# Kernel optimization log

Measured on AMD Instinct MI355X. Metric: run time of the kernel, lower is better.

Reference implementation:

```python
import jax, jax.numpy as jnp
import numpy as np

CAPACITY_FACTOR = 2  # GShard top-2 gating: C = 2*S/E


def setup_inputs() -> dict:
    key = jax.random.key(0)
    k1, k2, k3, k4 = jax.random.split(key, 4)
    B, T, M, E, F = 4, 1024, 1024, 8, 4096
    x = jax.random.normal(k1, (B, T, M), dtype=jnp.float32)
    wg = jax.random.normal(k2, (M, E), dtype=jnp.float32) * 0.02
    w1 = jax.random.normal(k3, (E, M, F), dtype=jnp.float32) * 0.02
    w2 = jax.random.normal(k4, (E, F, M), dtype=jnp.float32) * 0.02
    return {"x": x, "wg": wg, "w1": w1, "w2": w2}


def top2_gate(xs, wg):
    # xs: [S, M] tokens; wg: [M, E] gate projection.
    S = xs.shape[0]
    E = wg.shape[1]
    C = CAPACITY_FACTOR * S // E  # expert capacity
    logits = xs @ wg                                  # [S, E]
    gates = jax.nn.softmax(logits, axis=-1)           # [S, E]
    # top-1 expert
    idx1 = jnp.argmax(gates, axis=-1)                 # [S]
    mask1 = jax.nn.one_hot(idx1, E, dtype=jnp.int32)  # [S, E]
    # top-2 expert: mask out top-1 and take argmax again
    logits_no1 = jnp.where(mask1.astype(bool), -jnp.inf, logits)
    idx2 = jnp.argmax(logits_no1, axis=-1)
    mask2 = jax.nn.one_hot(idx2, E, dtype=jnp.int32)
    # positions within each expert's buffer (cumsum over tokens)
    loc1 = jnp.cumsum(mask1, axis=0) - 1              # [S, E]
    loc2 = jnp.cumsum(mask2, axis=0) - 1 + jnp.sum(mask1, axis=0, keepdims=True)
    # load-balancing auxiliary loss
    me = jnp.mean(gates, axis=0)
    ce = jnp.mean(mask1.astype(gates.dtype), axis=0)
    l_aux = jnp.mean(me * ce) * (E * E)
    # drop tokens beyond capacity
    mask1 = mask1 * (loc1 < C)
    mask2 = mask2 * (loc2 < C)
    loc1_s = jnp.sum(loc1 * mask1, axis=1)            # [S] slot of token in its top-1 expert
    loc2_s = jnp.sum(loc2 * mask2, axis=1)
    mask1f = mask1.astype(gates.dtype)
    mask2f = mask2.astype(gates.dtype)
    gates1_s = jnp.sum(gates * mask1f, axis=1)
    gates2_s = jnp.sum(gates * mask2f, axis=1)
    denom = gates1_s + gates2_s
    denom = jnp.where(denom < 1e-9, 1e-9, denom)
    g1 = gates1_s / denom
    g2 = gates2_s / denom
    # combine weights [S, E, C]
    combine = (g1[:, None] * mask1f)[:, :, None] * jax.nn.one_hot(loc1_s, C, dtype=gates.dtype)[:, None, :] \
            + (g2[:, None] * mask2f)[:, :, None] * jax.nn.one_hot(loc2_s, C, dtype=gates.dtype)[:, None, :]
    dispatch = (combine > 0).astype(gates.dtype)      # one-hot dispatch mask [S, E, C]
    return l_aux, combine, dispatch


def reference(x, wg, w1, w2):
    B, T, M = x.shape
    xs = x.reshape(-1, M)                                  # [S, M]
    l_aux, combine_weights, dispatch_mask = top2_gate(xs, wg)
    # dispatch: one-hot matmul (E*C x S) @ (S x M) -> [E, C, M]
    dispatched = jnp.einsum('sec,sm->ecm', dispatch_mask, xs)
    # per-expert FFN (relu)
    h = jax.nn.relu(jnp.einsum('ecm,emf->ecf', dispatched, w1))
    expert_out = jnp.einsum('ecf,efm->ecm', h, w2)         # [E, C, M]
    # combine: (S x E*C) @ (E*C x M) -> [S, M]
    combined = jnp.einsum('sec,ecm->sm', combine_weights, expert_out)
    return combined.reshape(B, T, M), l_aux
```

## Files before the change

kernel.cpp:

```cpp
#include <hip/hip_runtime.h>
#include <hip/hip_bf16.h>

typedef unsigned short u16;
typedef short bf16x8 __attribute__((ext_vector_type(8)));
typedef float f32x4 __attribute__((ext_vector_type(4)));
typedef u16 u16x8 __attribute__((ext_vector_type(8)));

#define S_TOK 4096
#define MDIM 1024
#define EDIM 8
#define FDIM 4096
#define CCAP 1024
#define HALF_F 2048

__device__ __align__(16) u16   g_xb [S_TOK * MDIM];
__device__ __align__(16) u16   g_wT [EDIM * FDIM * MDIM];
__device__ __align__(16) u16   g_h  [EDIM * CCAP * FDIM];
__device__ __align__(16) float g_eo [2 * EDIM * CCAP * MDIM];
__device__ float g_gates[S_TOK * EDIM];
__device__ int   g_idx1[S_TOK], g_idx2[S_TOK];
__device__ int   g_loc1[S_TOK], g_loc2[S_TOK];
__device__ float g_tg1[S_TOK],  g_tg2[S_TOK];
__device__ int   g_ts1[S_TOK],  g_ts2[S_TOK];
__device__ int   g_slot[EDIM * CCAP];

__device__ __forceinline__ u16 f2bf(float f) {
    union { float f; unsigned u; } c; c.f = f;
    unsigned r = c.u + 0x7FFFu + ((c.u >> 16) & 1u);
    return (u16)(r >> 16);
}
__device__ __forceinline__ void async16(const void* g, void* l) {
    __builtin_amdgcn_global_load_lds(
        (const __attribute__((address_space(1))) unsigned int*)g,
        (__attribute__((address_space(3))) unsigned int*)l, 16, 0, 0);
}

__global__ void cvt_x(const float* __restrict__ x) {
    int i = (blockIdx.x * 256 + threadIdx.x) * 8;
    float4 a = *(const float4*)(x + i);
    float4 b = *(const float4*)(x + i + 4);
    u16x8 o;
    o[0] = f2bf(a.x); o[1] = f2bf(a.y); o[2] = f2bf(a.z); o[3] = f2bf(a.w);
    o[4] = f2bf(b.x); o[5] = f2bf(b.y); o[6] = f2bf(b.z); o[7] = f2bf(b.w);
    *(u16x8*)(g_xb + i) = o;
}

__global__ void gate_kernel(const float* __restrict__ x, const float* __restrict__ wg) {
    __shared__ float wgT[EDIM * MDIM];
    const int tid = threadIdx.x, wave = tid >> 6, lane = tid & 63;
    for (int i = tid; i < EDIM * MDIM; i += 256) {
        int e = i >> 10, m = i & 1023;
        wgT[i] = wg[m * EDIM + e];
    }
    __syncthreads();
    const int s = blockIdx.x * 4 + wave;
    const float* xr = x + (size_t)s * MDIM;
    float lg[EDIM];
#pragma unroll
    for (int e = 0; e < EDIM; e++) lg[e] = 0.f;
#pragma unroll
    for (int j = 0; j < 4; j++) {
        int m0 = j * 256 + lane * 4;
        float4 xv = *(const float4*)(xr + m0);
#pragma unroll
        for (int e = 0; e < EDIM; e++) {
            float4 wv = *(const float4*)(&wgT[e * MDIM + m0]);
            lg[e] += xv.x * wv.x + xv.y * wv.y + xv.z * wv.z + xv.w * wv.w;
        }
    }
#pragma unroll
    for (int e = 0; e < EDIM; e++) {
        float v = lg[e];
        for (int o = 32; o >= 1; o >>= 1) v += __shfl_xor(v, o);
        lg[e] = v;
    }
    if (lane == 0) {
        float mx = lg[0];
#pragma unroll
        for (int e = 1; e < EDIM; e++) mx = fmaxf(mx, lg[e]);
        float ex[EDIM], sum = 0.f;
#pragma unroll
        for (int e = 0; e < EDIM; e++) { ex[e] = expf(lg[e] - mx); sum += ex[e]; }
        int i1 = 0; float b1 = lg[0];
#pragma unroll
        for (int e = 1; e < EDIM; e++) if (lg[e] > b1) { b1 = lg[e]; i1 = e; }
        int i2 = -1; float b2 = -3.4e38f;
#pragma unroll
        for (int e = 0; e < EDIM; e++) if (e != i1 && lg[e] > b2) { b2 = lg[e]; i2 = e; }
        float inv = 1.f / sum;
#pragma unroll
        for (int e = 0; e < EDIM; e++) g_gates[s * EDIM + e] = ex[e] * inv;
        g_idx1[s] = i1; g_idx2[s] = i2;
    }
}

__global__ void scan_kernel(float* __restrict__ out_laux) {
    __shared__ float me_sh[EDIM];
    __shared__ int cnt_sh[EDIM];
    const int t = threadIdx.x, wave = t >> 6, lane = t & 63;
    if (t < EDIM) { me_sh[t] = 0.f; cnt_sh[t] = 0; }
    for (int i = t; i < EDIM * CCAP; i += 1024) g_slot[i] = -1;
    __syncthreads();
    float lm[EDIM]; int lc[EDIM];
#pragma unroll
    for (int e = 0; e < EDIM; e++) { lm[e] = 0.f; lc[e] = 0; }
    for (int j = 0; j < 4; j++) {
        int s = t + 1024 * j;
        const float* g = g_gates + (size_t)s * EDIM;
        int i1 = g_idx1[s];
#pragma unroll
        for (int e = 0; e < EDIM; e++) { lm[e] += g[e]; lc[e] += (i1 == e); }
    }
#pragma unroll
    for (int e = 0; e < EDIM; e++) {
        float v = lm[e]; int c = lc[e];
        for (int o = 32; o >= 1; o >>= 1) { v += __shfl_xor(v, o); c += __shfl_xor(c, o); }
        if (lane == 0) { atomicAdd(&me_sh[e], v); atomicAdd(&cnt_sh[e], c); }
    }
    __syncthreads();
    {
        int e = wave & 7;
        const int* idx = (wave < 8) ? g_idx1 : g_idx2;
        int* loc = (wave < 8) ? g_loc1 : g_loc2;
        int running = (wave < 8) ? 0 : cnt_sh[e];
        for (int s0 = 0; s0 < S_TOK; s0 += 64) {
            int v = idx[s0 + lane];
            bool f = (v == e);
            unsigned long long m = __ballot(f);
            int rank = __popcll(m & ((1ull << lane) - 1ull));
            if (f) loc[s0 + lane] = running + rank;
            running += __popcll(m);
        }
    }
    __syncthreads();
    for (int j = 0; j < 4; j++) {
        int s = t + 1024 * j;
        int e1 = g_idx1[s], e2 = g_idx2[s];
        int l1 = g_loc1[s], l2 = g_loc2[s];
        bool k1 = l1 < CCAP, k2 = l2 < CCAP;
        float G1 = k1 ? g_gates[s * EDIM + e1] : 0.f;
        float G2 = k2 ? g_gates[s * EDIM + e2] : 0.f;
        float den = G1 + G2; den = den < 1e-9f ? 1e-9f : den;
        g_tg1[s] = G1 / den; g_tg2[s] = G2 / den;
        g_ts1[s] = k1 ? (e1 * CCAP + l1) : -1;
        g_ts2[s] = k2 ? (e2 * CCAP + l2) : -1;
        if (k1) g_slot[e1 * CCAP + l1] = s;
        if (k2) g_slot[e2 * CCAP + l2] = s;
    }
    if (t == 0) {
        float la = 0.f;
        for (int e = 0; e < EDIM; e++)
            la += (me_sh[e] / (float)S_TOK) * ((float)cnt_sh[e] / (float)S_TOK);
        la *= (float)EDIM;
        out_laux[0] = la;
    }
}

template <int R, int C>
__global__ void transpose_cvt(const float* __restrict__ in) {
    __shared__ __align__(16) u16 t[64][72];
    const float* I = in + (size_t)blockIdx.z * R * C;
    u16* O = g_wT + (size_t)blockIdx.z * R * C;
    const int tid = threadIdx.x;
    const int c0 = blockIdx.x * 64, r0 = blockIdx.y * 64;
    const int rr = tid >> 4;
    const int cc = (tid & 15) * 4;
#pragma unroll
    for (int j = 0; j < 4; j++) {
        int r = rr + j * 16;
        float4 v = *(const float4*)(I + (size_t)(r0 + r) * C + c0 + cc);
        t[cc + 0][r] = f2bf(v.x);
        t[cc + 1][r] = f2bf(v.y);
        t[cc + 2][r] = f2bf(v.z);
        t[cc + 3][r] = f2bf(v.w);
    }
    __syncthreads();
    const int oc = tid >> 2;
    const int orr = (tid & 3) * 16;
    u16x8 a = *(const u16x8*)(&t[oc][orr]);
    u16x8 b = *(const u16x8*)(&t[oc][orr + 8]);
    u16* dst = O + (size_t)(c0 + oc) * R + r0 + orr;
    *(u16x8*)(dst) = a;
    *(u16x8*)(dst + 8) = b;
}

__global__ void gemm_gather() {
    constexpr int K = MDIM, N = FDIM;
    __shared__ __align__(16) u16 As[128 * 32];
    __shared__ __align__(16) u16 Bs[128 * 32];
    const int tid = threadIdx.x, wave = tid >> 6, lane = tid & 63;
    const int e = blockIdx.z, qr = tid >> 2, qc = tid & 3;
    const int sb = e * CCAP + blockIdx.y * 128;
    int t0 = g_slot[sb + qr];      if (t0 < 0) t0 = 0;
    int t1 = g_slot[sb + 64 + qr]; if (t1 < 0) t1 = 0;
    const u16* ga0 = g_xb + (size_t)t0 * K + qc * 8;
    const u16* ga1 = g_xb + (size_t)t1 * K + qc * 8;
    const u16* B = g_wT + (size_t)e * N * K + (size_t)(blockIdx.x * 128) * K;
    const u16* gb0 = B + (size_t)qr * K + qc * 8;
    const u16* gb1 = gb0 + (size_t)64 * K;
    u16* lA0 = As + wave * 512;
    u16* lA1 = As + 2048 + wave * 512;
    u16* lB0 = Bs + wave * 512;
    u16* lB1 = Bs + 2048 + wave * 512;

    f32x4 acc[4][4];
#pragma unroll
    for (int i = 0; i < 4; i++)
#pragma unroll
        for (int j = 0; j < 4; j++) { f32x4 z = {0.f, 0.f, 0.f, 0.f}; acc[i][j] = z; }
    const int wm = (wave >> 1) * 64, wn = (wave & 1) * 64;
    const int lrow = lane & 15, lq = lane >> 4;

    for (int k0 = 0; k0 < K; k0 += 32) {
        __syncthreads();
        async16(ga0, lA0); async16(ga1, lA1);
        async16(gb0, lB0); async16(gb1, lB1);
        ga0 += 32; ga1 += 32; gb0 += 32; gb1 += 32;
        __syncthreads();
        bf16x8 af[4], bfr[4];
#pragma unroll
    for (int i = 0; i < 4; i++)
            af[i] = *(const bf16x8*)(As + (wm + i * 16 + lrow) * 32 + lq * 8);
#pragma unroll
        for (int i = 0; i < 4; i++)
            bfr[i] = *(const bf16x8*)(Bs + (wn + i * 16 + lrow) * 32 + lq * 8);
#pragma unroll
        for (int mi = 0; mi < 4; mi++)
#pragma unroll
            for (int ni = 0; ni < 4; ni++)
                acc[mi][ni] = __builtin_amdgcn_mfma_f32_16x16x32_bf16(
                    af[mi], bfr[ni], acc[mi][ni], 0, 0, 0);
    }
    const int r0 = blockIdx.y * 128 + wm + lq * 4;
    const int c0 = blockIdx.x * 128 + wn + lrow;
    u16* D = g_h + (size_t)e * CCAP * N;
#pragma unroll
    for (int mi = 0; mi < 4; mi++)
#pragma unroll
        for (int v = 0; v < 4; v++) {
            size_t r = (size_t)(r0 + mi * 16 + v) * N;
#pragma unroll
            for (int ni = 0; ni < 4; ni++) {
                float xv = acc[mi][ni][v];
                xv = xv > 0.f ? xv : 0.f;
                D[r + c0 + ni * 16] = f2bf(xv);
            }
        }
}

__global__ void gemm_bt() {
    constexpr int LD = FDIM;
    constexpr int K = HALF_F;
    constexpr int N = MDIM;
    __shared__ __align__(16) u16 As[128 * 32];
    __shared__ __align__(16) u16 Bs[128 * 32];
    const int tid = threadIdx.x, wave = tid >> 6, lane = tid & 63;
    const int e = blockIdx.z >> 1, ks = blockIdx.z & 1;
    const int qr = tid >> 2, qc = tid & 3;
    const u16* A = g_h + (size_t)e * CCAP * LD + (size_t)(blockIdx.y * 128) * LD + ks * K;
    const u16* B = g_wT + (size_t)e * N * LD + (size_t)(blockIdx.x * 128) * LD + ks * K;
    const u16* ga0 = A + (size_t)qr * LD + qc * 8;
    const u16* ga1 = ga0 + (size_t)64 * LD;
    const u16* gb0 = B + (size_t)qr * LD + qc * 8;
    const u16* gb1 = gb0 + (size_t)64 * LD;
    u16* lA0 = As + wave * 512;
    u16* lA1 = As + 2048 + wave * 512;
    u16* lB0 = Bs + wave * 512;
    u16* lB1 = Bs + 2048 + wave * 512;

    f32x4 acc[4][4];
#pragma unroll
    for (int i = 0; i < 4; i++)
#pragma unroll
        for (int j = 0; j < 4; j++) { f32x4 z = {0.f, 0.f, 0.f, 0.f}; acc[i][j] = z; }
    const int wm = (wave >> 1) * 64, wn = (wave & 1) * 64;
    const int lrow = lane & 15, lq = lane >> 4;

    for (int k0 = 0; k0 < K; k0 += 32) {
        __syncthreads();
        async16(ga0, lA0); async16(ga1, lA1);
        async16(gb0, lB0); async16(gb1, lB1);
        ga0 += 32; ga1 += 32; gb0 += 32; gb1 += 32;
        __syncthreads();
        bf16x8 af[4], bfr[4];
#pragma unroll
        for (int i = 0; i < 4; i++)
            af[i] = *(const bf16x8*)(As + (wm + i * 16 + lrow) * 32 + lq * 8);
#pragma unroll
        for (int i = 0; i < 4; i++)
            bfr[i] = *(const bf16x8*)(Bs + (wn + i * 16 + lrow) * 32 + lq * 8);
#pragma unroll
        for (int mi = 0; mi < 4; mi++)
#pragma unroll
            for (int ni = 0; ni < 4; ni++)
                acc[mi][ni] = __builtin_amdgcn_mfma_f32_16x16x32_bf16(
                    af[mi], bfr[ni], acc[mi][ni], 0, 0, 0);
    }
    const int r0 = blockIdx.y * 128 + wm + lq * 4;
    const int c0 = blockIdx.x * 128 + wn + lrow;
    float* D = g_eo + (size_t)ks * (EDIM * CCAP * MDIM) + (size_t)e * CCAP * N;
#pragma unroll
    for (int mi = 0; mi < 4; mi++)
#pragma unroll
        for (int v = 0; v < 4; v++) {
            size_t r = (size_t)(r0 + mi * 16 + v) * N;
#pragma unroll
            for (int ni = 0; ni < 4; ni++)
                D[r + c0 + ni * 16] = acc[mi][ni][v];
        }
}

__global__ void combine_kernel(float* __restrict__ out) {
    const int s = blockIdx.x, t = threadIdx.x;
    constexpr size_t HALF = (size_t)EDIM * CCAP * MDIM;
    float g1 = g_tg1[s], g2 = g_tg2[s];
    int p1 = g_ts1[s], p2 = g_ts2[s];
    float a0 = 0.f, a1 = 0.f, a2 = 0.f, a3 = 0.f;
    if (p1 >= 0) {
        float4 v = ((const float4*)(g_eo + (size_t)p1 * MDIM))[t];
        float4 w = ((const float4*)(g_eo + HALF + (size_t)p1 * MDIM))[t];
        a0 = g1 * (v.x + w.x); a1 = g1 * (v.y + w.y);
        a2 = g1 * (v.z + w.z); a3 = g1 * (v.w + w.w);
    }
    if (p2 >= 0) {
        float4 v = ((const float4*)(g_eo + (size_t)p2 * MDIM))[t];
        float4 w = ((const float4*)(g_eo + HALF + (size_t)p2 * MDIM))[t];
        a0 += g2 * (v.x + w.x); a1 += g2 * (v.y + w.y);
        a2 += g2 * (v.z + w.z); a3 += g2 * (v.w + w.w);
    }
    float4 o; o.x = a0; o.y = a1; o.z = a2; o.w = a3;
    ((float4*)out)[(size_t)s * 256 + t] = o;
}

extern "C" void kernel_launch(void* const* d_in, const int* in_sizes, int n_in,
                              void* d_out, int out_size, void* d_ws, size_t ws_size,
                              hipStream_t stream) {
    const float* x  = (const float*)d_in[0];
    const float* wg = (const float*)d_in[1];
    const float* w1 = (const float*)d_in[2];
    const float* w2 = (const float*)d_in[3];
    float* out = (float*)d_out;

    cvt_x<<<dim3(S_TOK * MDIM / 2048), 256, 0, stream>>>(x);
    gate_kernel<<<dim3(S_TOK / 4), 256, 0, stream>>>(x, wg);
    scan_kernel<<<dim3(1), 1024, 0, stream>>>(out + 4194304);

    transpose_cvt<MDIM, FDIM><<<dim3(FDIM / 64, MDIM / 64, EDIM), 256, 0, stream>>>(w1);
    gemm_gather<<<dim3(FDIM / 128, CCAP / 128, EDIM), 256, 0, stream>>>();

    transpose_cvt<FDIM, MDIM><<<dim3(MDIM / 64, FDIM / 64, EDIM), 256, 0, stream>>>(w2);
    gemm_bt<<<dim3(MDIM / 128, CCAP / 128, EDIM * 2), 256, 0, stream>>>();

    combine_kernel<<<dim3(S_TOK), 256, 0, stream>>>(out);
}
```

Baseline: 555.1 us.

## Double-buffer LDS in expert GEMMs with XOR swizzle and XCD-aware block remap

Both expert GEMMs now use two LDS buffers, so async global-to-LDS loads for the next K-slice are issued while MFMAs run on the current one. The explicit vmcnt waits and raw barriers replace the two __syncthreads per iteration. An XOR swizzle on LDS columns is meant to cut bank conflicts, and s_setprio raises wave priority around the MFMA block. Blocks are launched on a 1D grid and remapped so neighbouring tiles land on the same XCD for L2 reuse. Doubled LDS use and the launch bounds may limit occupancy, and the hand-written waitcnt counts must match the issued loads exactly.

```diff
diff --git a/kernel.cpp b/kernel.cpp
--- a/kernel.cpp
+++ b/kernel.cpp
@@ -184,24 +184,68 @@
     *(u16x8*)(dst + 8) = b;
 }
 
-__global__ void gemm_gather() {
-    constexpr int K = MDIM, N = FDIM;
-    __shared__ __align__(16) u16 As[128 * 32];
-    __shared__ __align__(16) u16 Bs[128 * 32];
+#define GSTAGE(sA, sB)                                                      \
+    {                                                                       \
+        async16(gA0, sA + stA0); async16(gA1, sA + stA1);                   \
+        async16(gB0, sB + stA0); async16(gB1, sB + stA1);                   \
+        gA0 += 32; gA1 += 32; gB0 += 32; gB1 += 32;                         \
+    }
+
+#define GCOMPUTE(sA, sB)                                                    \
+    {                                                                       \
+        bf16x8 af[4], bfr[4];                                               \
+        _Pragma("unroll")                                                   \
+        for (int i = 0; i < 4; i++) {                                       \
+            af[i]  = *(const bf16x8*)(sA + (wm + i * 16 + lrow) * 32 + cr); \
+            bfr[i] = *(const bf16x8*)(sB + (wn + i * 16 + lrow) * 32 + cr); \
+        }                                                                   \
+        __builtin_amdgcn_s_setprio(1);                                      \
+        _Pragma("unroll")                                                   \
+        for (int mi = 0; mi < 4; mi++)                                      \
+            _Pragma("unroll")                                               \
+            for (int ni = 0; ni < 4; ni++)                                  \
+                acc[mi][ni] = __builtin_amdgcn_mfma_f32_16x16x32_bf16(      \
+                    af[mi], bfr[ni], acc[mi][ni], 0, 0, 0);                 \
+        __builtin_amdgcn_s_setprio(0);                                      \
+    }
+
+#define WAIT4 asm volatile("s_waitcnt vmcnt(4)" ::: "memory")
+#define WAIT0 asm volatile("s_waitcnt vmcnt(0)" ::: "memory")
+#define BAR   __builtin_amdgcn_s_barrier()
+
+#define GEMM_PIPELINE(T)                                                    \
+    GSTAGE(As0, Bs0);                                                       \
+    GSTAGE(As1, Bs1);                                                       \
+    for (int t = 0; t < (T) - 2; t += 2) {                                  \
+        WAIT4; BAR;                                                         \
+        GCOMPUTE(As0, Bs0);                                                 \
+        BAR;                                                                \
+        GSTAGE(As0, Bs0);                                                   \
+        WAIT4; BAR;                                                         \
+        GCOMPUTE(As1, Bs1);                                                 \
+        BAR;                                                                \
+        GSTAGE(As1, Bs1);                                                   \
+    }                                                                       \
+    WAIT4; BAR;                                                             \
+    GCOMPUTE(As0, Bs0);                                                     \
+    WAIT0; BAR;                                                             \
+    GCOMPUTE(As1, Bs1);
+
+__global__ __launch_bounds__(256, 4) void gemm_gather() {
+    __shared__ __align__(16) u16 As0[4096], As1[4096], Bs0[4096], Bs1[4096];
     const int tid = threadIdx.x, wave = tid >> 6, lane = tid & 63;
-    const int e = blockIdx.z, qr = tid >> 2, qc = tid & 3;
-    const int sb = e * CCAP + blockIdx.y * 128;
-    int t0 = g_slot[sb + qr];      if (t0 < 0) t0 = 0;
-    int t1 = g_slot[sb + 64 + qr]; if (t1 < 0) t1 = 0;
-    const u16* ga0 = g_xb + (size_t)t0 * K + qc * 8;
-    const u16* ga1 = g_xb + (size_t)t1 * K + qc * 8;
-    const u16* B = g_wT + (size_t)e * N * K + (size_t)(blockIdx.x * 128) * K;
-    const u16* gb0 = B + (size_t)qr * K + qc * 8;
-    const u16* gb1 = gb0 + (size_t)64 * K;
-    u16* lA0 = As + wave * 512;
-    u16* lA1 = As + 2048 + wave * 512;
-    u16* lB0 = Bs + wave * 512;
-    u16* lB1 = Bs + 2048 + wave * 512;
+    const int id = (blockIdx.x & 7) * 256 + (blockIdx.x >> 3);
+    const int by = id & 7, bx = (id >> 3) & 31, e = id >> 8;
+    const int scol = (((lane & 3) ^ ((lane >> 3) & 3)) * 8);
+    const int stA0 = wave * 512, stA1 = 2048 + wave * 512;
+    const int sb = e * CCAP + by * 128;
+    int s0 = g_slot[sb + wave * 16 + (lane >> 2)];      if (s0 < 0) s0 = 0;
+    int s1 = g_slot[sb + 64 + wave * 16 + (lane >> 2)]; if (s1 < 0) s1 = 0;
+    const u16* gA0 = g_xb + (size_t)s0 * MDIM + scol;
+    const u16* gA1 = g_xb + (size_t)s1 * MDIM + scol;
+    const u16* Bb = g_wT + ((size_t)e * FDIM + bx * 128) * MDIM;
+    const u16* gB0 = Bb + (size_t)(wave * 16 + (lane >> 2)) * MDIM + scol;
+    const u16* gB1 = gB0 + (size_t)64 * MDIM;
 
     f32x4 acc[4][4];
 #pragma unroll
@@ -210,35 +254,18 @@
         for (int j = 0; j < 4; j++) { f32x4 z = {0.f, 0.f, 0.f, 0.f}; acc[i][j] = z; }
     const int wm = (wave >> 1) * 64, wn = (wave & 1) * 64;
     const int lrow = lane & 15, lq = lane >> 4;
-
-    for (int k0 = 0; k0 < K; k0 += 32) {
-        __syncthreads();
-        async16(ga0, lA0); async16(ga1, lA1);
-        async16(gb0, lB0); async16(gb1, lB1);
-        ga0 += 32; ga1 += 32; gb0 += 32; gb1 += 32;
-        __syncthreads();
-        bf16x8 af[4], bfr[4];
-#pragma unroll
-    for (int i = 0; i < 4; i++)
-            af[i] = *(const bf16x8*)(As + (wm + i * 16 + lrow) * 32 + lq * 8);
-#pragma unroll
-        for (int i = 0; i < 4; i++)
-            bfr[i] = *(const bf16x8*)(Bs + (wn + i * 16 + lrow) * 32 + lq * 8);
-#pragma unroll
-        for (int mi = 0; mi < 4; mi++)
-#pragma unroll
-            for (int ni = 0; ni < 4; ni++)
-                acc[mi][ni] = __builtin_amdgcn_mfma_f32_16x16x32_bf16(
-                    af[mi], bfr[ni], acc[mi][ni], 0, 0, 0);
-    }
-    const int r0 = blockIdx.y * 128 + wm + lq * 4;
-    const int c0 = blockIdx.x * 128 + wn + lrow;
-    u16* D = g_h + (size_t)e * CCAP * N;
+    const int cr = ((lq ^ ((lrow >> 1) & 3)) * 8);
+
+    GEMM_PIPELINE(MDIM / 32)
+
+    const int r0 = by * 128 + wm + lq * 4;
+    const int c0 = bx * 128 + wn + lrow;
+    u16* D = g_h + (size_t)e * CCAP * FDIM;
 #pragma unroll
     for (int mi = 0; mi < 4; mi++)
 #pragma unroll
         for (int v = 0; v < 4; v++) {
-            size_t r = (size_t)(r0 + mi * 16 + v) * N;
+            size_t r = (size_t)(r0 + mi * 16 + v) * FDIM;
 #pragma unroll
             for (int ni = 0; ni < 4; ni++) {
                 float xv = acc[mi][ni][v];
@@ -248,62 +275,40 @@
         }
 }
 
-__global__ void gemm_bt() {
-    constexpr int LD = FDIM;
-    constexpr int K = HALF_F;
-    constexpr int N = MDIM;
-    __shared__ __align__(16) u16 As[128 * 32];
-    __shared__ __align__(16) u16 Bs[128 * 32];
+__global__ __launch_bounds__(256, 4) void gemm_bt() {
+    __shared__ __align__(16) u16 As0[4096], As1[4096], Bs0[4096], Bs1[4096];
     const int tid = threadIdx.x, wave = tid >> 6, lane = tid & 63;
-    const int e = blockIdx.z >> 1, ks = blockIdx.z & 1;
-    const int qr = tid >> 2, qc = tid & 3;
-    const u16* A = g_h + (size_t)e * CCAP * LD + (size_t)(blockIdx.y * 128) * LD + ks * K;
-    const u16* B = g_wT + (size_t)e * N * LD + (size_t)(blockIdx.x * 128) * LD + ks * K;
-    const u16* ga0 = A + (size_t)qr * LD + qc * 8;
-    const u16* ga1 = ga0 + (size_t)64 * LD;
-    const u16* gb0 = B + (size_t)qr * LD + qc * 8;
-    const u16* gb1 = gb0 + (size_t)64 * LD;
-    u16* lA0 = As + wave * 512;
-    u16* lA1 = As + 2048 + wave * 512;
-    u16* lB0 = Bs + wave * 512;
-    u16* lB1 = Bs + 2048 + wave * 512;
+    const int id = (blockIdx.x & 7) * 128 + (blockIdx.x >> 3);
+    const int by = id & 7, bx = (id >> 3) & 7, z = id >> 6;
+    const int e = z >> 1, ks = z & 1;
+    const int scol = (((lane & 3) ^ ((lane >> 3) & 3)) * 8);
+    const int stA0 = wave * 512, stA1 = 2048 + wave * 512;
+    const u16* Ab = g_h + (size_t)e * CCAP * FDIM + (size_t)(by * 128) * FDIM + ks * HALF_F;
+    const u16* Bb = g_wT + (size_t)e * MDIM * FDIM + (size_t)(bx * 128) * FDIM + ks * HALF_F;
+    const u16* gA0 = Ab + (size_t)(wave * 16 + (lane >> 2)) * FDIM + scol;
+    const u16* gA1 = gA0 + (size_t)64 * FDIM;
+    const u16* gB0 = Bb + (size_t)(wave * 16 + (lane >> 2)) * FDIM + scol;
+    const u16* gB1 = gB0 + (size_t)64 * FDIM;
 
     f32x4 acc[4][4];
 #pragma unroll
     for (int i = 0; i < 4; i++)
 #pragma unroll
-        for (int j = 0; j < 4; j++) { f32x4 z = {0.f, 0.f, 0.f, 0.f}; acc[i][j] = z; }
+        for (int j = 0; j < 4; j++) { f32x4 z2 = {0.f, 0.f, 0.f, 0.f}; acc[i][j] = z2; }
     const int wm = (wave >> 1) * 64, wn = (wave & 1) * 64;
     const int lrow = lane & 15, lq = lane >> 4;
-
-    for (int k0 = 0; k0 < K; k0 += 32) {
-        __syncthreads();
-        async16(ga0, lA0); async16(ga1, lA1);
-        async16(gb0, lB0); async16(gb1, lB1);
-        ga0 += 32; ga1 += 32; gb0 += 32; gb1 += 32;
-        __syncthreads();
-        bf16x8 af[4], bfr[4];
-#pragma unroll
-        for (int i = 0; i < 4; i++)
-            af[i] = *(const bf16x8*)(As + (wm + i * 16 + lrow) * 32 + lq * 8);
-#pragma unroll
-        for (int i = 0; i < 4; i++)
-            bfr[i] = *(const bf16x8*)(Bs + (wn + i * 16 + lrow) * 32 + lq * 8);
-#pragma unroll
-        for (int mi = 0; mi < 4; mi++)
-#pragma unroll
-            for (int ni = 0; ni < 4; ni++)
-                acc[mi][ni] = __builtin_amdgcn_mfma_f32_16x16x32_bf16(
-                    af[mi], bfr[ni], acc[mi][ni], 0, 0, 0);
-    }
-    const int r0 = blockIdx.y * 128 + wm + lq * 4;
-    const int c0 = blockIdx.x * 128 + wn + lrow;
-    float* D = g_eo + (size_t)ks * (EDIM * CCAP * MDIM) + (size_t)e * CCAP * N;
+    const int cr = ((lq ^ ((lrow >> 1) & 3)) * 8);
+
+    GEMM_PIPELINE(HALF_F / 32)
+
+    const int r0 = by * 128 + wm + lq * 4;
+    const int c0 = bx * 128 + wn + lrow;
+    float* D = g_eo + (size_t)ks * (EDIM * CCAP * MDIM) + (size_t)e * CCAP * MDIM;
 #pragma unroll
     for (int mi = 0; mi < 4; mi++)
 #pragma unroll
         for (int v = 0; v < 4; v++) {
-            size_t r = (size_t)(r0 + mi * 16 + v) * N;
+            size_t r = (size_t)(r0 + mi * 16 + v) * MDIM;
 #pragma unroll
             for (int ni = 0; ni < 4; ni++)
                 D[r + c0 + ni * 16] = acc[mi][ni][v];
@@ -346,10 +351,10 @@
     scan_kernel<<<dim3(1), 1024, 0, stream>>>(out + 4194304);
 
     transpose_cvt<MDIM, FDIM><<<dim3(FDIM / 64, MDIM / 64, EDIM), 256, 0, stream>>>(w1);
-    gemm_gather<<<dim3(FDIM / 128, CCAP / 128, EDIM), 256, 0, stream>>>();
+    gemm_gather<<<dim3(2048), 256, 0, stream>>>();
 
     transpose_cvt<FDIM, MDIM><<<dim3(MDIM / 64, FDIM / 64, EDIM), 256, 0, stream>>>(w2);
-    gemm_bt<<<dim3(MDIM / 128, CCAP / 128, EDIM * 2), 256, 0, stream>>>();
+    gemm_bt<<<dim3(1024), 256, 0, stream>>>();
 
     combine_kernel<<<dim3(S_TOK), 256, 0, stream>>>(out);
 }
```

Measured after the change: 537.3 us. -3.2%, faster.
